# Kernel tuning notes

Hardware: AMD Instinct MI355X
Metric: run time of the kernel (lower is better)

Reference implementation:

```python
import jax, jax.numpy as jnp
import numpy as np

N, A, C, S = 65536, 1024, 1000, 2  # S = max aug multiplier from self.augs


def _update_cv(x, labels, cov_prior, ave_prior, amount_prior):
    # Efficient segment-reduce form of update_CV (original builds O(N*C*A) onehot tensor)
    cnt = jax.ops.segment_sum(jnp.ones((N,), x.dtype), labels, num_segments=C)  # [C]
    sum_c = jax.ops.segment_sum(x, labels, num_segments=C)                      # [C,A]
    cnt_c = jnp.where(cnt == 0, 1.0, cnt)                                       # Amount_CxA clamp
    ave = sum_c / cnt_c[:, None]                                                # ave_CxA
    var = jax.ops.segment_sum((x - ave[labels]) ** 2, labels, num_segments=C) / cnt_c[:, None]
    var = jnp.where(var == 0, 1e-10, var)
    w = (cnt / (cnt + amount_prior + 1e-10))[:, None]                           # weight_CV [C,1]
    additional = w * (1 - w) * (ave_prior - ave) ** 2
    new_cov = cov_prior * (1 - w) + var * w + additional
    new_ave = ave_prior * (1 - w) + ave * w
    new_amount = amount_prior + cnt
    return new_cov, new_ave, new_amount


def setup_inputs() -> dict:
    key = jax.random.key(0)
    ks = jax.random.split(key, 6)
    return {
        "x": jax.random.normal(ks[0], (N, A), jnp.float32),
        "eps": jax.random.normal(ks[1], (S, C, A), jnp.float32),
        "fc_w": jax.random.normal(ks[2], (C, A), jnp.float32) * 0.02,
        "fc_b": jnp.zeros((C,), jnp.float32),
        "ba_coeffi": jax.random.normal(ks[3], (C,), jnp.float32) * 0.1,
        "cov_prior": jax.random.uniform(ks[4], (C, A), jnp.float32) * 0.01,
        "ave_prior": jnp.zeros((C, A), jnp.float32),
        "amount_prior": jnp.zeros((C,), jnp.float32),
        "target_x": jax.random.randint(ks[5], (N,), 0, C).astype(jnp.int64),
    }


def reference(x, eps, fc_w, fc_b, ba_coeffi, cov_prior, ave_prior, amount_prior, target_x):
    # update_CV runs under torch.no_grad -> stop_gradient on stats
    new_cov, new_ave, _ = _update_cv(x, target_x, cov_prior, ave_prior, amount_prior)
    new_cov = jax.lax.stop_gradient(new_cov)
    new_ave = jax.lax.stop_gradient(new_ave)
    # Gaussian augmentation: Normal(loc=Ave, scale=CoVariance).sample((S,)) per class
    aug = new_ave[None, :, :] + new_cov[None, :, :] * eps  # [S,C,A]
    aug = aug.reshape(S * C, A)
    aug_labels = jnp.tile(jnp.arange(C, dtype=target_x.dtype), S)
    feats = jnp.concatenate([x, aug], axis=0)              # [N+S*C, A]
    labels_all = jnp.concatenate([target_x, aug_labels], axis=0)
    logits = feats @ fc_w.T + fc_b - ba_coeffi             # [N+S*C, C]
    logp = jax.nn.log_softmax(logits, axis=-1)
    loss = -jnp.mean(jnp.take_along_axis(logp, labels_all[:, None], axis=1))
    return loss
```

## Files before the change

kernel.cpp:

```cpp
#include <hip/hip_runtime.h>

#define NROWS 65536
#define ADIM  1024
#define CCLS  1000
#define SAUG  2
#define MROWS (NROWS + SAUG*CCLS)
#define MPAD  67584
#define NPAD  1024
#define NPART 8
#define NEG_INF (-3.0e38f)

typedef __bf16 bf16x8 __attribute__((ext_vector_type(8)));
typedef float  f32x4  __attribute__((ext_vector_type(4)));
typedef unsigned short u16;

__device__ __forceinline__ unsigned pk2bf(float a, float b){
  unsigned ua = __float_as_uint(a), ub = __float_as_uint(b);
  ua = (ua + 0x7FFFu + ((ua>>16)&1u)) >> 16;
  ub = (ub + 0x7FFFu + ((ub>>16)&1u)) >> 16;
  return ua | (ub<<16);
}
__device__ __forceinline__ float bflo(unsigned u){ return __uint_as_float((u & 0xFFFFu) << 16); }
__device__ __forceinline__ float bfhi(unsigned u){ return __uint_as_float(u & 0xFFFF0000u); }

__global__ void k_hist(const int* __restrict__ tgt, int* __restrict__ cnt){
  int i = blockIdx.x*blockDim.x + threadIdx.x;
  int stride = gridDim.x*blockDim.x;
  for (; i < NROWS; i += stride) atomicAdd(&cnt[tgt[i]], 1);
}

__global__ void k_scan(const int* __restrict__ cnt, int* __restrict__ start){
  __shared__ int s[1024];
  int t = threadIdx.x;
  int v = (t < CCLS) ? cnt[t] : 0;
  s[t] = v;
  __syncthreads();
  for (int off = 1; off < 1024; off <<= 1){
    int u = (t >= off) ? s[t-off] : 0;
    __syncthreads();
    s[t] += u;
    __syncthreads();
  }
  if (t < CCLS) start[t] = s[t] - v;
}

__global__ void k_scatter(const int* __restrict__ tgt, const int* __restrict__ start,
                          int* __restrict__ pos, int* __restrict__ sorted){
  int i = blockIdx.x*blockDim.x + threadIdx.x;
  int stride = gridDim.x*blockDim.x;
  for (; i < NROWS; i += stride){
    int c = tgt[i];
    int r = atomicAdd(&pos[c], 1);
    sorted[start[c] + r] = i;
  }
}

__global__ void k_cvt_x(const float* __restrict__ x, u16* __restrict__ xb){
  size_t i = ((size_t)blockIdx.x*blockDim.x + threadIdx.x)*8;
  float4 a = *(const float4*)(x+i);
  float4 b = *(const float4*)(x+i+4);
  uint4 o;
  o.x = pk2bf(a.x,a.y); o.y = pk2bf(a.z,a.w);
  o.z = pk2bf(b.x,b.y); o.w = pk2bf(b.z,b.w);
  *(uint4*)(xb+i) = o;
}

__global__ void k_pad(u16* __restrict__ xb){
  size_t i = ((size_t)blockIdx.x*blockDim.x + threadIdx.x)*8 + (size_t)MROWS*ADIM;
  uint4 z = {0u,0u,0u,0u};
  *(uint4*)(xb+i) = z;
}

__global__ void k_cvt_w(const float* __restrict__ w, u16* __restrict__ wb){
  size_t i = ((size_t)blockIdx.x*blockDim.x + threadIdx.x)*8;
  int row = (int)(i >> 10);
  uint4 o = {0u,0u,0u,0u};
  if (row < CCLS){
    float4 a = *(const float4*)(w+i);
    float4 b = *(const float4*)(w+i+4);
    o.x = pk2bf(a.x,a.y); o.y = pk2bf(a.z,a.w);
    o.z = pk2bf(b.x,b.y); o.w = pk2bf(b.z,b.w);
  }
  *(uint4*)(wb+i) = o;
}

__global__ void k_bias(const float* __restrict__ fc_b, const float* __restrict__ ba,
                       float* __restrict__ biasv){
  int c = blockIdx.x*blockDim.x + threadIdx.x;
  if (c < NPAD) biasv[c] = (c < CCLS) ? fc_b[c] - ba[c] : NEG_INF;
}

__global__ void k_stats(const u16* __restrict__ xb_in, const int* __restrict__ sorted,
                        const int* __restrict__ cnt, const int* __restrict__ start,
                        const float* __restrict__ amt_p, const float* __restrict__ cov_p,
                        const float* __restrict__ ave_p, const float* __restrict__ eps,
                        u16* __restrict__ xb){
  int c = blockIdx.x;
  int t = threadIdx.x;
  int col = t*4;
  int n = cnt[c];
  int st = start[c];
  float s[4] = {0.f,0.f,0.f,0.f}, q[4] = {0.f,0.f,0.f,0.f};
  for (int i = 0; i < n; i++){
    int row = sorted[st + i];
    const uint2 uv = *(const uint2*)(xb_in + (size_t)row*ADIM + col);
    float v0 = bflo(uv.x), v1 = bfhi(uv.x), v2 = bflo(uv.y), v3 = bfhi(uv.y);
    s[0]+=v0; s[1]+=v1; s[2]+=v2; s[3]+=v3;
    q[0]+=v0*v0; q[1]+=v1*v1; q[2]+=v2*v2; q[3]+=v3*v3;
  }
  float cf = (float)n;
  float cc = (n == 0) ? 1.f : cf;
  float wgt = cf / (cf + amt_p[c] + 1e-10f);
  float4 cv = *(const float4*)(cov_p + (size_t)c*ADIM + col);
  float4 av = *(const float4*)(ave_p + (size_t)c*ADIM + col);
  float cvp[4] = {cv.x,cv.y,cv.z,cv.w};
  float avp[4] = {av.x,av.y,av.z,av.w};
  float ncov[4], nave[4];
  #pragma unroll
  for (int j = 0; j < 4; j++){
    float ave = s[j]/cc;
    float var = (q[j] - 2.f*ave*s[j] + cf*ave*ave)/cc;
    if (var <= 0.f) var = 1e-10f;
    float add = wgt*(1.f-wgt)*(avp[j]-ave)*(avp[j]-ave);
    ncov[j] = cvp[j]*(1.f-wgt) + var*wgt + add;
    nave[j] = avp[j]*(1.f-wgt) + ave*wgt;
  }
  #pragma unroll
  for (int s_ = 0; s_ < SAUG; s_++){
    size_t eoff = ((size_t)(s_*CCLS + c))*ADIM + col;
    size_t roff = ((size_t)(NROWS + s_*CCLS + c))*ADIM + col;
    const float4 e = *(const float4*)(eps + eoff);
    uint2 o;
    o.x = pk2bf(nave[0]+ncov[0]*e.x, nave[1]+ncov[1]*e.y);
    o.y = pk2bf(nave[2]+ncov[2]*e.z, nave[3]+ncov[3]*e.w);
    *(uint2*)(xb + roff) = o;
  }
}

__global__ __launch_bounds__(256,2) void k_gemm_part(
    const u16* __restrict__ xb, const u16* __restrict__ wb,
    const float* __restrict__ biasv, const int* __restrict__ tgt,
    float* __restrict__ pm, float* __restrict__ pl, float* __restrict__ plab){
  __shared__ char smem[24576] __attribute__((aligned(16)));
  char* smA = smem;
  char* smB = smem + 8192;
  const int t = threadIdx.x;
  const int lane = t & 63;
  const int wv = t >> 6;
  const int rh = wv & 1;
  const int ch = wv >> 1;
  const int quad = lane >> 4;
  const int col = lane & 15;
  const int row0 = blockIdx.y * 128;
  const int sp = blockIdx.x;

  f32x4 acc[4][8];
  const f32x4 z = {0.f,0.f,0.f,0.f};
  #pragma unroll
  for (int sm = 0; sm < 4; sm++)
    #pragma unroll
    for (int sn = 0; sn < 8; sn++) acc[sm][sn] = z;

  const u16* ga = xb + (size_t)row0*ADIM;
  const u16* gb = wb + (size_t)(sp*256)*ADIM;

  for (int kc = 0; kc < ADIM/32; kc++){
    __syncthreads();
    #pragma unroll
    for (int i = 0; i < 2; i++){
      int o = wv*2048 + i*1024 + lane*16;
      const u16* g = ga + (size_t)(o>>6)*ADIM + kc*32 + ((o>>4)&3)*8;
      __builtin_amdgcn_global_load_lds((const __attribute__((address_space(1))) void*)g,
          (__attribute__((address_space(3))) void*)(smA + wv*2048 + i*1024), 16, 0, 0);
    }
    #pragma unroll
    for (int i = 0; i < 4; i++){
      int o = wv*4096 + i*1024 + lane*16;
      const u16* g = gb + (size_t)(o>>6)*ADIM + kc*32 + ((o>>4)&3)*8;
      __builtin_amdgcn_global_load_lds((const __attribute__((address_space(1))) void*)g,
          (__attribute__((address_space(3))) void*)(smB + wv*4096 + i*1024), 16, 0, 0);
    }
    __syncthreads();
    bf16x8 af[4], bfr[8];
    const int kq = quad*16;
    #pragma unroll
    for (int sm = 0; sm < 4; sm++){
      int r = rh*64 + sm*16 + col;
      af[sm] = *(const bf16x8*)(smA + r*64 + kq);
    }
    #pragma unroll
    for (int sn = 0; sn < 8; sn++){
      int n = ch*128 + sn*16 + col;
      bfr[sn] = *(const bf16x8*)(smB + n*64 + kq);
    }
    #pragma unroll
    for (int sm = 0; sm < 4; sm++)
      #pragma unroll
      for (int sn = 0; sn < 8; sn++)
        acc[sm][sn] = __builtin_amdgcn_mfma_f32_16x16x32_bf16(af[sm], bfr[sn], acc[sm][sn], 0, 0, 0);
  }

  float bias[8];
  #pragma unroll
  for (int sn = 0; sn < 8; sn++) bias[sn] = biasv[sp*256 + ch*128 + sn*16 + col];
  #pragma unroll
  for (int i = 0; i < 16; i++){
    const int sm = i>>2, rg = i&3;
    const int gr = row0 + rh*64 + sm*16 + quad*4 + rg;
    int lbl = -1;
    if (gr < NROWS) lbl = tgt[gr];
    else if (gr < MROWS){ int a = gr - NROWS; lbl = (a < CCLS) ? a : a - CCLS; }
    float lg[8];
    float mx = NEG_INF, lv = NEG_INF;
    #pragma unroll
    for (int sn = 0; sn < 8; sn++){
      float v = acc[sm][sn][rg] + bias[sn];
      lg[sn] = v;
      mx = fmaxf(mx, v);
      int c = sp*256 + ch*128 + sn*16 + col;
      lv = (c == lbl) ? v : lv;
    }
    #pragma unroll
    for (int o = 1; o < 16; o <<= 1) mx = fmaxf(mx, __shfl_xor(mx, o));
    float se = 0.f;
    #pragma unroll
    for (int sn = 0; sn < 8; sn++) se += __expf(lg[sn] - mx);
    #pragma unroll
    for (int o = 1; o < 16; o <<= 1) se += __shfl_xor(se, o);
    #pragma unroll
    for (int o = 1; o < 16; o <<= 1) lv = fmaxf(lv, __shfl_xor(lv, o));
    if (col == 0){
      size_t idx = (size_t)(sp*2 + ch)*MPAD + gr;
      pm[idx]   = mx;
      pl[idx]   = se;
      plab[idx] = lv;
    }
  }
}

__global__ void k_merge(const float* __restrict__ pm, const float* __restrict__ pl,
                        const float* __restrict__ plab, float* __restrict__ out){
  int r = blockIdx.x*256 + threadIdx.x;
  float v = 0.f;
  if (r < MROWS){
    float m = NEG_INF, lb = NEG_INF;
    #pragma unroll
    for (int s = 0; s < NPART; s++){
      m  = fmaxf(m,  pm[(size_t)s*MPAD + r]);
      lb = fmaxf(lb, plab[(size_t)s*MPAD + r]);
    }
    float l = 0.f;
    #pragma unroll
    for (int s = 0; s < NPART; s++)
      l += pl[(size_t)s*MPAD + r]*__expf(pm[(size_t)s*MPAD + r] - m);
    v = (m + __logf(l) - lb) * (1.0f/(float)MROWS);
  }
  #pragma unroll
  for (int o = 32; o > 0; o >>= 1) v += __shfl_xor(v, o);
  if ((threadIdx.x & 63) == 0) atomicAdd(out, v);
}

extern "C" void kernel_launch(void* const* d_in, const int* in_sizes, int n_in,
                              void* d_out, int out_size, void* d_ws, size_t ws_size,
                              hipStream_t stream) {
  const float* x     = (const float*)d_in[0];
  const float* eps   = (const float*)d_in[1];
  const float* fc_w  = (const float*)d_in[2];
  const float* fc_b  = (const float*)d_in[3];
  const float* ba    = (const float*)d_in[4];
  const float* cov_p = (const float*)d_in[5];
  const float* ave_p = (const float*)d_in[6];
  const float* amt_p = (const float*)d_in[7];
  const int*   tgt   = (const int*)d_in[8];
  float* out = (float*)d_out;

  char* ws = (char*)d_ws;
  u16*   xb    = (u16*)(ws);
  u16*   wb    = (u16*)(ws + 138412032u);
  float* biasv = (float*)(ws + 140509184u);
  int*   sorted= (int*)(ws + 140513280u);
  int*   cnt   = (int*)(ws + 140775424u);
  int*   pos   = (int*)(ws + 140779520u);
  int*   start = (int*)(ws + 140783616u);
  float* pm    = (float*)(ws + 140787712u);
  float* pl    = (float*)(ws + 142950400u);
  float* plab  = (float*)(ws + 145113088u);

  hipMemsetAsync(cnt, 0, 12288, stream);
  hipMemsetAsync(out, 0, sizeof(float), stream);

  k_hist   <<<256, 256, 0, stream>>>(tgt, cnt);
  k_scan   <<<1, 1024, 0, stream>>>(cnt, start);
  k_scatter<<<256, 256, 0, stream>>>(tgt, start, pos, sorted);
  k_cvt_x  <<<32768, 256, 0, stream>>>(x, xb);
  k_pad    <<<24, 256, 0, stream>>>(xb);
  k_cvt_w  <<<512, 256, 0, stream>>>(fc_w, wb);
  k_bias   <<<4, 256, 0, stream>>>(fc_b, ba, biasv);
  k_stats  <<<CCLS, 256, 0, stream>>>(xb, sorted, cnt, start, amt_p, cov_p, ave_p, eps, xb);
  k_gemm_part<<<dim3(4, 528), 256, 0, stream>>>(xb, wb, biasv, tgt, pm, pl, plab);
  k_merge  <<<264, 256, 0, stream>>>(pm, pl, plab, out);
}
```

Measured before the change: 698.3 us.

## Restructure GEMM into 256x256 tiles with 4-stage async LDS pipeline

Rewrites the fused GEMM+softmax-partial kernel to use 512-thread blocks computing 256x256 tiles, with a 4-deep ring of LDS buffers fed by global_load_lds prefetches issued three K-steps ahead. LDS addresses get an XOR swizzle to cut bank conflicts, and the block ID is remapped so neighbouring blocks share weight tiles. The four column-wave partials are reduced in LDS before writing, which halves the partition count the merge kernel reads. The price is 128KB of dynamic shared memory per block and hand-scheduled inline asm waits that depend on exact instruction counts.

```diff
diff --git a/kernel.cpp b/kernel.cpp
--- a/kernel.cpp
+++ b/kernel.cpp
@@ -7,7 +7,7 @@
 #define MROWS (NROWS + SAUG*CCLS)
 #define MPAD  67584
 #define NPAD  1024
-#define NPART 8
+#define NPART 4
 #define NEG_INF (-3.0e38f)
 
 typedef __bf16 bf16x8 __attribute__((ext_vector_type(8)));
@@ -137,104 +137,197 @@
   }
 }
 
-__global__ __launch_bounds__(256,2) void k_gemm_part(
+__global__ __launch_bounds__(512,2) void k_gemm_part(
     const u16* __restrict__ xb, const u16* __restrict__ wb,
     const float* __restrict__ biasv, const int* __restrict__ tgt,
     float* __restrict__ pm, float* __restrict__ pl, float* __restrict__ plab){
-  __shared__ char smem[24576] __attribute__((aligned(16)));
-  char* smA = smem;
-  char* smB = smem + 8192;
+  extern __shared__ char smem[];
   const int t = threadIdx.x;
   const int lane = t & 63;
   const int wv = t >> 6;
-  const int rh = wv & 1;
-  const int ch = wv >> 1;
+  const int wr = wv >> 2;
+  const int wc = wv & 3;
+  const int col = lane & 15;
   const int quad = lane >> 4;
-  const int col = lane & 15;
-  const int row0 = blockIdx.y * 128;
-  const int sp = blockIdx.x;
-
-  f32x4 acc[4][8];
+
+  const int bid = blockIdx.x;
+  const int wg  = (bid & 7)*132 + (bid >> 3);
+  const int sp  = wg & 3;
+  const int row0 = (wg >> 2) * 256;
+
+  const unsigned lds0 = (unsigned)(size_t)((__attribute__((address_space(3))) char*)smem);
+
+  unsigned aoff[8], boff[4];
+  #pragma unroll
+  for (int m = 0; m < 8; m++){
+    unsigned lin = (unsigned)((wr*128 + m*16 + col)*64 + quad*16);
+    aoff[m] = lds0 + (lin ^ (((lin >> 7) & 3u) << 4));
+  }
+  #pragma unroll
+  for (int n = 0; n < 4; n++){
+    unsigned lin = (unsigned)((wc*64 + n*16 + col)*64 + quad*16);
+    boff[n] = lds0 + 16384u + (lin ^ (((lin >> 7) & 3u) << 4));
+  }
+
+  const u16* src[4];
+  int dstoff[4];
+  {
+    const u16* gA = xb + (size_t)row0*ADIM;
+    const u16* gB = wb + (size_t)(sp*256)*ADIM;
+    #pragma unroll
+    for (int j = 0; j < 4; j++){
+      unsigned d = (unsigned)((j & 1)*8192 + wv*1024 + lane*16);
+      unsigned s = d ^ ((((unsigned)lane >> 3) & 3u) << 4);
+      src[j] = (j < 2 ? gA : gB) + (size_t)(s >> 6)*ADIM + ((s & 63u) >> 1);
+      dstoff[j] = (j < 2 ? 0 : 16384) + (j & 1)*8192 + wv*1024;
+    }
+  }
+
+#define STG(tile, nb, j) \
+  __builtin_amdgcn_global_load_lds( \
+      (const __attribute__((address_space(1))) void*)(src[j] + (size_t)(tile)*32), \
+      (__attribute__((address_space(3))) void*)(smem + (nb)*32768 + dstoff[j]), 16, 0, 0)
+
+  f32x4 acc[8][4];
   const f32x4 z = {0.f,0.f,0.f,0.f};
   #pragma unroll
-  for (int sm = 0; sm < 4; sm++)
-    #pragma unroll
-    for (int sn = 0; sn < 8; sn++) acc[sm][sn] = z;
-
-  const u16* ga = xb + (size_t)row0*ADIM;
-  const u16* gb = wb + (size_t)(sp*256)*ADIM;
-
-  for (int kc = 0; kc < ADIM/32; kc++){
-    __syncthreads();
-    #pragma unroll
-    for (int i = 0; i < 2; i++){
-      int o = wv*2048 + i*1024 + lane*16;
-      const u16* g = ga + (size_t)(o>>6)*ADIM + kc*32 + ((o>>4)&3)*8;
-      __builtin_amdgcn_global_load_lds((const __attribute__((address_space(1))) void*)g,
-          (__attribute__((address_space(3))) void*)(smA + wv*2048 + i*1024), 16, 0, 0);
+  for (int m = 0; m < 8; m++)
+    #pragma unroll
+    for (int n = 0; n < 4; n++) acc[m][n] = z;
+
+  #pragma unroll
+  for (int p = 0; p < 3; p++){
+    STG(p, p, 0); STG(p, p, 1); STG(p, p, 2); STG(p, p, 3);
+  }
+
+  for (int kt = 0; kt < 29; kt++){
+    const int cb = kt & 3, nb = (kt + 3) & 3;
+    const unsigned cbo = (unsigned)(cb << 15);
+    bf16x8 af[4], bfr[4];
+    STG(kt+3, nb, 0); STG(kt+3, nb, 1);
+    asm volatile("s_waitcnt vmcnt(10)" ::: "memory");
+    __builtin_amdgcn_sched_barrier(0);
+    __builtin_amdgcn_s_barrier();
+    __builtin_amdgcn_sched_barrier(0);
+    #pragma unroll
+    for (int m = 0; m < 4; m++)
+      asm volatile("ds_read_b128 %0, %1" : "=v"(af[m]) : "v"(aoff[m]+cbo));
+    #pragma unroll
+    for (int n = 0; n < 4; n++)
+      asm volatile("ds_read_b128 %0, %1" : "=v"(bfr[n]) : "v"(boff[n]+cbo));
+    asm volatile("s_waitcnt lgkmcnt(0)" ::: "memory");
+    __builtin_amdgcn_sched_barrier(0);
+    __builtin_amdgcn_s_setprio(1);
+    #pragma unroll
+    for (int m = 0; m < 4; m++)
+      #pragma unroll
+      for (int n = 0; n < 4; n++)
+        acc[m][n] = __builtin_amdgcn_mfma_f32_16x16x32_bf16(af[m], bfr[n], acc[m][n], 0, 0, 0);
+    __builtin_amdgcn_s_setprio(0);
+    STG(kt+3, nb, 2); STG(kt+3, nb, 3);
+    #pragma unroll
+    for (int m = 0; m < 4; m++)
+      asm volatile("ds_read_b128 %0, %1" : "=v"(af[m]) : "v"(aoff[4+m]+cbo));
+    asm volatile("s_waitcnt lgkmcnt(0)" ::: "memory");
+    __builtin_amdgcn_sched_barrier(0);
+    __builtin_amdgcn_s_setprio(1);
+    #pragma unroll
+    for (int m = 0; m < 4; m++)
+      #pragma unroll
+      for (int n = 0; n < 4; n++)
+        acc[4+m][n] = __builtin_amdgcn_mfma_f32_16x16x32_bf16(af[m], bfr[n], acc[4+m][n], 0, 0, 0);
+    __builtin_amdgcn_s_setprio(0);
+    __builtin_amdgcn_sched_barrier(0);
+    __builtin_amdgcn_s_barrier();
+  }
+
+  asm volatile("s_waitcnt vmcnt(0)" ::: "memory");
+  __builtin_amdgcn_sched_barrier(0);
+  __builtin_amdgcn_s_barrier();
+  #pragma unroll
+  for (int kt = 29; kt < 32; kt++){
+    const unsigned cbo = (unsigned)((kt & 3) << 15);
+    bf16x8 af[4], bfr[4];
+    #pragma unroll
+    for (int m = 0; m < 4; m++)
+      asm volatile("ds_read_b128 %0, %1" : "=v"(af[m]) : "v"(aoff[m]+cbo));
+    #pragma unroll
+    for (int n = 0; n < 4; n++)
+      asm volatile("ds_read_b128 %0, %1" : "=v"(bfr[n]) : "v"(boff[n]+cbo));
+    asm volatile("s_waitcnt lgkmcnt(0)" ::: "memory");
+    __builtin_amdgcn_sched_barrier(0);
+    #pragma unroll
+    for (int m = 0; m < 4; m++)
+      #pragma unroll
+      for (int n = 0; n < 4; n++)
+        acc[m][n] = __builtin_amdgcn_mfma_f32_16x16x32_bf16(af[m], bfr[n], acc[m][n], 0, 0, 0);
+    #pragma unroll
+    for (int m = 0; m < 4; m++)
+      asm volatile("ds_read_b128 %0, %1" : "=v"(af[m]) : "v"(aoff[4+m]+cbo));
+    asm volatile("s_waitcnt lgkmcnt(0)" ::: "memory");
+    __builtin_amdgcn_sched_barrier(0);
+    #pragma unroll
+    for (int m = 0; m < 4; m++)
+      #pragma unroll
+      for (int n = 0; n < 4; n++)
+        acc[4+m][n] = __builtin_amdgcn_mfma_f32_16x16x32_bf16(af[m], bfr[n], acc[4+m][n], 0, 0, 0);
+  }
+#undef STG
+
+  float bias[4];
+  #pragma unroll
+  for (int n = 0; n < 4; n++) bias[n] = biasv[sp*256 + wc*64 + n*16 + col];
+
+  __syncthreads();
+  float* red = (float*)smem;
+
+  #pragma unroll
+  for (int m = 0; m < 8; m++){
+    #pragma unroll
+    for (int rg = 0; rg < 4; rg++){
+      const int rb = wr*128 + m*16 + quad*4 + rg;
+      const int gr = row0 + rb;
+      int lbl = -1;
+      if (gr < NROWS) lbl = tgt[gr];
+      else if (gr < MROWS){ int a_ = gr - NROWS; lbl = (a_ < CCLS) ? a_ : a_ - CCLS; }
+      float lg[4];
+      float mx = NEG_INF, lv = NEG_INF;
+      #pragma unroll
+      for (int n = 0; n < 4; n++){
+        float v = acc[m][n][rg] + bias[n];
+        lg[n] = v;
+        mx = fmaxf(mx, v);
+        int c = sp*256 + wc*64 + n*16 + col;
+        lv = (c == lbl) ? v : lv;
+      }
+      #pragma unroll
+      for (int o = 1; o < 16; o <<= 1) mx = fmaxf(mx, __shfl_xor(mx, o));
+      float se = 0.f;
+      #pragma unroll
+      for (int n = 0; n < 4; n++) se += __expf(lg[n] - mx);
+      #pragma unroll
+      for (int o = 1; o < 16; o <<= 1) se += __shfl_xor(se, o);
+      #pragma unroll
+      for (int o = 1; o < 16; o <<= 1) lv = fmaxf(lv, __shfl_xor(lv, o));
+      if (col == 0){
+        red[0*1024 + rb*4 + wc] = mx;
+        red[1*1024 + rb*4 + wc] = se;
+        red[2*1024 + rb*4 + wc] = lv;
+      }
     }
-    #pragma unroll
-    for (int i = 0; i < 4; i++){
-      int o = wv*4096 + i*1024 + lane*16;
-      const u16* g = gb + (size_t)(o>>6)*ADIM + kc*32 + ((o>>4)&3)*8;
-      __builtin_amdgcn_global_load_lds((const __attribute__((address_space(1))) void*)g,
-          (__attribute__((address_space(3))) void*)(smB + wv*4096 + i*1024), 16, 0, 0);
-    }
-    __syncthreads();
-    bf16x8 af[4], bfr[8];
-    const int kq = quad*16;
-    #pragma unroll
-    for (int sm = 0; sm < 4; sm++){
-      int r = rh*64 + sm*16 + col;
-      af[sm] = *(const bf16x8*)(smA + r*64 + kq);
-    }
-    #pragma unroll
-    for (int sn = 0; sn < 8; sn++){
-      int n = ch*128 + sn*16 + col;
-      bfr[sn] = *(const bf16x8*)(smB + n*64 + kq);
-    }
-    #pragma unroll
-    for (int sm = 0; sm < 4; sm++)
-      #pragma unroll
-      for (int sn = 0; sn < 8; sn++)
-        acc[sm][sn] = __builtin_amdgcn_mfma_f32_16x16x32_bf16(af[sm], bfr[sn], acc[sm][sn], 0, 0, 0);
-  }
-
-  float bias[8];
-  #pragma unroll
-  for (int sn = 0; sn < 8; sn++) bias[sn] = biasv[sp*256 + ch*128 + sn*16 + col];
-  #pragma unroll
-  for (int i = 0; i < 16; i++){
-    const int sm = i>>2, rg = i&3;
-    const int gr = row0 + rh*64 + sm*16 + quad*4 + rg;
-    int lbl = -1;
-    if (gr < NROWS) lbl = tgt[gr];
-    else if (gr < MROWS){ int a = gr - NROWS; lbl = (a < CCLS) ? a : a - CCLS; }
-    float lg[8];
-    float mx = NEG_INF, lv = NEG_INF;
-    #pragma unroll
-    for (int sn = 0; sn < 8; sn++){
-      float v = acc[sm][sn][rg] + bias[sn];
-      lg[sn] = v;
-      mx = fmaxf(mx, v);
-      int c = sp*256 + ch*128 + sn*16 + col;
-      lv = (c == lbl) ? v : lv;
-    }
-    #pragma unroll
-    for (int o = 1; o < 16; o <<= 1) mx = fmaxf(mx, __shfl_xor(mx, o));
-    float se = 0.f;
-    #pragma unroll
-    for (int sn = 0; sn < 8; sn++) se += __expf(lg[sn] - mx);
-    #pragma unroll
-    for (int o = 1; o < 16; o <<= 1) se += __shfl_xor(se, o);
-    #pragma unroll
-    for (int o = 1; o < 16; o <<= 1) lv = fmaxf(lv, __shfl_xor(lv, o));
-    if (col == 0){
-      size_t idx = (size_t)(sp*2 + ch)*MPAD + gr;
-      pm[idx]   = mx;
-      pl[idx]   = se;
-      plab[idx] = lv;
-    }
+  }
+  __syncthreads();
+  if (t < 256){
+    float m0 = red[t*4+0], m1 = red[t*4+1], m2 = red[t*4+2], m3 = red[t*4+3];
+    float mx = fmaxf(fmaxf(m0,m1), fmaxf(m2,m3));
+    float l  = red[1024+t*4+0]*__expf(m0-mx) + red[1024+t*4+1]*__expf(m1-mx)
+             + red[1024+t*4+2]*__expf(m2-mx) + red[1024+t*4+3]*__expf(m3-mx);
+    float lv = fmaxf(fmaxf(red[2048+t*4+0],red[2048+t*4+1]),
+                     fmaxf(red[2048+t*4+2],red[2048+t*4+3]));
+    size_t idx = (size_t)sp*MPAD + (size_t)(row0 + t);
+    pm[idx]   = mx;
+    pl[idx]   = l;
+    plab[idx] = lv;
   }
 }
 
@@ -286,6 +379,13 @@
   float* pl    = (float*)(ws + 142950400u);
   float* plab  = (float*)(ws + 145113088u);
 
+  static int cfg = 0;
+  if (!cfg){
+    hipFuncSetAttribute((const void*)k_gemm_part,
+                        hipFuncAttributeMaxDynamicSharedMemorySize, 131072);
+    cfg = 1;
+  }
+
   hipMemsetAsync(cnt, 0, 12288, stream);
   hipMemsetAsync(out, 0, sizeof(float), stream);
 
@@ -297,6 +397,6 @@
   k_cvt_w  <<<512, 256, 0, stream>>>(fc_w, wb);
   k_bias   <<<4, 256, 0, stream>>>(fc_b, ba, biasv);
   k_stats  <<<CCLS, 256, 0, stream>>>(xb, sorted, cnt, start, amt_p, cov_p, ave_p, eps, xb);
-  k_gemm_part<<<dim3(4, 528), 256, 0, stream>>>(xb, wb, biasv, tgt, pm, pl, plab);
+  k_gemm_part<<<1056, 512, 131072, stream>>>(xb, wb, biasv, tgt, pm, pl, plab);
   k_merge  <<<264, 256, 0, stream>>>(pm, pl, plab, out);
 }
```

After: 705.9 us. About the same (+1.1%).
